# Optimization experiments

Hardware: AMD Instinct MI355X
Metric: run time of the kernel (lower is better)

## Reference

```python
import jax, jax.numpy as jnp
import numpy as np

H = 16
D_MODEL = 1024
D_K = D_MODEL // H
NWORDS = 16384


def setup_inputs() -> dict:
    key0 = jax.random.key(0)
    ks = jax.random.split(key0, 11)
    s = 0.02
    return {
        "query": jax.random.normal(ks[0], (1, D_MODEL), dtype=jnp.float32),
        "key": jax.random.normal(ks[1], (NWORDS, D_MODEL), dtype=jnp.float32),
        "value": jax.random.normal(ks[2], (NWORDS, D_MODEL), dtype=jnp.float32),
        "Wq": jax.random.normal(ks[3], (D_MODEL, D_MODEL), dtype=jnp.float32) * s,
        "bq": jax.random.normal(ks[4], (D_MODEL,), dtype=jnp.float32) * s,
        "Wk": jax.random.normal(ks[5], (D_MODEL, D_MODEL), dtype=jnp.float32) * s,
        "bk": jax.random.normal(ks[6], (D_MODEL,), dtype=jnp.float32) * s,
        "Wv": jax.random.normal(ks[7], (D_MODEL, D_MODEL), dtype=jnp.float32) * s,
        "bv": jax.random.normal(ks[8], (D_MODEL,), dtype=jnp.float32) * s,
        "Wo": jax.random.normal(ks[9], (D_MODEL, D_MODEL), dtype=jnp.float32) * s,
        "bo": jax.random.normal(ks[10], (D_MODEL,), dtype=jnp.float32) * s,
    }


def reference(query, key, value, Wq, bq, Wk, bk, Wv, bv, Wo, bo):
    # torch Linear: y = x @ W.T + b
    q = (query @ Wq.T + bq).reshape(H, D_K)          # [h, d_k]  (single query token)
    k = (key @ Wk.T + bk).reshape(-1, H, D_K)        # [n, h, d_k]
    v = (value @ Wv.T + bv).reshape(-1, H, D_K)      # [n, h, d_k]
    # NOTE: original module applies NO 1/sqrt(d_k) scaling.
    scores = jnp.einsum("hd,nhd->hn", q, k)          # [h, n]
    p_attn = jax.nn.softmax(scores, axis=-1)          # dropout p=0 -> no-op
    x = jnp.einsum("hn,nhd->hd", p_attn, v).reshape(1, H * D_K)  # [1, d_model]
    return x @ Wo.T + bo                              # [1, d_model]
```

## Files before the change

kernel.cpp:

```cpp
#include <hip/hip_runtime.h>

#define DM 1024
#define NW 16384

#define OFF_Q    0
#define OFF_C    1024
#define OFF_D0   17408
#define OFF_S    17424
#define OFF_X    17696
#define OFF_W    18720
#define OFF_E    36864
#define OFF_PART 299008

__global__ __launch_bounds__(256) void k_rowdot(const float* __restrict__ W,
                                                const float* __restrict__ v,
                                                const float* __restrict__ b,
                                                float* __restrict__ out) {
  const int wave = (blockIdx.x * 256 + threadIdx.x) >> 6;
  const int lane = threadIdx.x & 63;
  const float* row = W + (size_t)wave * DM + 4 * lane;
  float s = 0.f;
#pragma unroll
  for (int j = 0; j < 4; ++j) {
    float4 a = *(const float4*)(row + j * 256);
    float4 x = *(const float4*)(v + j * 256 + 4 * lane);
    s += a.x * x.x + a.y * x.y + a.z * x.z + a.w * x.w;
  }
#pragma unroll
  for (int off = 32; off; off >>= 1) s += __shfl_xor(s, off, 64);
  if (lane == 0) out[wave] = s + b[wave];
}

__global__ __launch_bounds__(256) void k_ck(const float* __restrict__ Wk,
                                            const float* __restrict__ bk,
                                            const float* __restrict__ q,
                                            float* __restrict__ c,
                                            float* __restrict__ d0) {
  const int h = blockIdx.x >> 2;
  const int mc = blockIdx.x & 3;
  const int m = mc * 256 + threadIdx.x;
  __shared__ float qh[64];
  if (threadIdx.x < 64) qh[threadIdx.x] = q[h * 64 + threadIdx.x];
  __syncthreads();
  const float* Wp = Wk + (size_t)(h * 64) * DM + m;
  float s = 0.f;
#pragma unroll 8
  for (int d = 0; d < 64; ++d) s += qh[d] * Wp[(size_t)d * DM];
  c[h * DM + m] = s;
  if (mc == 0 && threadIdx.x == 0) {
    float t = 0.f;
    for (int d = 0; d < 64; ++d) t += qh[d] * bk[h * 64 + d];
    d0[h] = t;
  }
}

__global__ __launch_bounds__(256, 3) void k_scores(const float* __restrict__ key,
                                                   const float* __restrict__ c,
                                                   const float* __restrict__ d0,
                                                   float* __restrict__ e,
                                                   float* __restrict__ S) {
  const int lane = threadIdx.x & 63;
  const int wv = threadIdx.x >> 6;
  const int hbase = wv * 4;
  const int n0 = blockIdx.x * 16;
  float4 cf[4][4];
#pragma unroll
  for (int hh = 0; hh < 4; ++hh)
#pragma unroll
    for (int j = 0; j < 4; ++j)
      cf[hh][j] = *(const float4*)(c + (size_t)(hbase + hh) * DM + j * 256 + 4 * lane);
  const int hl = (lane >> 4) & 3;
  const float dh = d0[hbase + hl];
  const bool hi5 = (lane & 32) != 0;
  const bool hi4 = (lane & 16) != 0;
  const bool writer = (lane & 15) == 0;
  float Ssum = 0.f;
  for (int r = 0; r < 16; ++r) {
    const int n = n0 + r;
    const float* kp = key + (size_t)n * DM + 4 * lane;
    float4 k0 = *(const float4*)(kp + 0);
    float4 k1 = *(const float4*)(kp + 256);
    float4 k2 = *(const float4*)(kp + 512);
    float4 k3 = *(const float4*)(kp + 768);
    float s[4];
#pragma unroll
    for (int hh = 0; hh < 4; ++hh) {
      s[hh] = cf[hh][0].x * k0.x + cf[hh][0].y * k0.y + cf[hh][0].z * k0.z + cf[hh][0].w * k0.w
            + cf[hh][1].x * k1.x + cf[hh][1].y * k1.y + cf[hh][1].z * k1.z + cf[hh][1].w * k1.w
            + cf[hh][2].x * k2.x + cf[hh][2].y * k2.y + cf[hh][2].z * k2.z + cf[hh][2].w * k2.w
            + cf[hh][3].x * k3.x + cf[hh][3].y * k3.y + cf[hh][3].z * k3.z + cf[hh][3].w * k3.w;
    }
    float keep0 = hi5 ? s[2] : s[0], send0 = hi5 ? s[0] : s[2];
    float v0 = keep0 + __shfl_xor(send0, 32, 64);
    float keep1 = hi5 ? s[3] : s[1], send1 = hi5 ? s[1] : s[3];
    float v1 = keep1 + __shfl_xor(send1, 32, 64);
    float keep = hi4 ? v1 : v0, send = hi4 ? v0 : v1;
    float t = keep + __shfl_xor(send, 16, 64);
    t += __shfl_xor(t, 8, 64);
    t += __shfl_xor(t, 4, 64);
    t += __shfl_xor(t, 2, 64);
    t += __shfl_xor(t, 1, 64);
    t = __expf(t + dh);
    if (writer) {
      e[(size_t)n * 16 + hbase + hl] = t;
      Ssum += t;
    }
  }
  if (writer) atomicAdd(S + (size_t)(hbase + hl) * 16, Ssum);
}

__global__ __launch_bounds__(256, 4) void k_pv(const float* __restrict__ value,
                                               const float* __restrict__ e,
                                               float* __restrict__ part) {
  const int nb = blockIdx.x >> 2;
  const int mc = blockIdx.x & 3;
  const int col = mc * 256 + threadIdx.x;
  const int n0 = nb * 128;
  float acc[16];
#pragma unroll
  for (int h = 0; h < 16; ++h) acc[h] = 0.f;
  const float* vp = value + (size_t)n0 * DM + col;
  const float* ep = e + (size_t)n0 * 16;
#pragma unroll 2
  for (int r = 0; r < 128; ++r) {
    float v = vp[(size_t)r * DM];
    const float* __restrict__ er = ep + r * 16;
#pragma unroll
    for (int h = 0; h < 16; ++h) acc[h] = fmaf(er[h], v, acc[h]);
  }
  float* pp = part + (size_t)nb * (16 * DM) + col;
#pragma unroll
  for (int h = 0; h < 16; ++h) pp[(size_t)h * DM] = acc[h];
}

__global__ __launch_bounds__(256) void k_wred(const float* __restrict__ part,
                                              float* __restrict__ w) {
  const int o = blockIdx.x * 256 + threadIdx.x;
  float s = 0.f;
#pragma unroll 8
  for (int nb = 0; nb < 128; ++nb) s += part[(size_t)nb * 16384 + o];
  w[o] = s;
}

__global__ __launch_bounds__(256) void k_xproj(const float* __restrict__ Wv,
                                               const float* __restrict__ w,
                                               const float* __restrict__ bv,
                                               const float* __restrict__ S,
                                               float* __restrict__ x) {
  const int wave = (blockIdx.x * 256 + threadIdx.x) >> 6;
  const int lane = threadIdx.x & 63;
  const int h = wave >> 6;
  const float* vec = w + (size_t)h * DM;
  const float* row = Wv + (size_t)wave * DM + 4 * lane;
  float s = 0.f;
#pragma unroll
  for (int j = 0; j < 4; ++j) {
    float4 a = *(const float4*)(row + j * 256);
    float4 x4 = *(const float4*)(vec + j * 256 + 4 * lane);
    s += a.x * x4.x + a.y * x4.y + a.z * x4.z + a.w * x4.w;
  }
#pragma unroll
  for (int off = 32; off; off >>= 1) s += __shfl_xor(s, off, 64);
  if (lane == 0) x[wave] = s / S[(size_t)h * 16] + bv[wave];
}

extern "C" void kernel_launch(void* const* d_in, const int* in_sizes, int n_in,
                              void* d_out, int out_size, void* d_ws, size_t ws_size,
                              hipStream_t stream) {
  const float* query = (const float*)d_in[0];
  const float* key   = (const float*)d_in[1];
  const float* value = (const float*)d_in[2];
  const float* Wq    = (const float*)d_in[3];
  const float* bq    = (const float*)d_in[4];
  const float* Wk    = (const float*)d_in[5];
  const float* bk    = (const float*)d_in[6];
  const float* Wv    = (const float*)d_in[7];
  const float* bv    = (const float*)d_in[8];
  const float* Wo    = (const float*)d_in[9];
  const float* bo    = (const float*)d_in[10];
  float* out = (float*)d_out;
  float* ws  = (float*)d_ws;

  hipMemsetAsync(ws + OFF_S, 0, 256 * sizeof(float), stream);
  k_rowdot <<<256, 256, 0, stream>>>(Wq, query, bq, ws + OFF_Q);
  k_ck     <<<64,  256, 0, stream>>>(Wk, bk, ws + OFF_Q, ws + OFF_C, ws + OFF_D0);
  k_scores <<<1024,256, 0, stream>>>(key, ws + OFF_C, ws + OFF_D0, ws + OFF_E, ws + OFF_S);
  k_pv     <<<512, 256, 0, stream>>>(value, ws + OFF_E, ws + OFF_PART);
  k_wred   <<<64,  256, 0, stream>>>(ws + OFF_PART, ws + OFF_W);
  k_xproj  <<<256, 256, 0, stream>>>(Wv, ws + OFF_W, bv, ws + OFF_S, ws + OFF_X);
  k_rowdot <<<256, 256, 0, stream>>>(Wo, ws + OFF_X, bo, out);
}
```

Baseline: 247.1 us.

## Fuse Q projection into c-vector kernel, restructure PV tiling, widen reduction

Folds the Wq projection and the S zeroing into the k_ck kernel, removing a memset and one launch, though each of the 64 blocks now recomputes its head's 64 q entries. The PV kernel switches to float4 columns with four waves each covering 32 rows of a 128-row chunk, reduced through shared memory, so value loads are wider and the e reads are amortised over four columns. The partial-sum reduction uses four threads per output with shuffle combining, giving 256 blocks instead of 64 for more parallelism.

Result: slower. 259.9 us (+5.1%).

```diff
diff --git a/kernel.cpp b/kernel.cpp
--- a/kernel.cpp
+++ b/kernel.cpp
@@ -3,7 +3,6 @@
 #define DM 1024
 #define NW 16384
 
-#define OFF_Q    0
 #define OFF_C    1024
 #define OFF_D0   17408
 #define OFF_S    17424
@@ -31,26 +30,50 @@
   if (lane == 0) out[wave] = s + b[wave];
 }
 
-__global__ __launch_bounds__(256) void k_ck(const float* __restrict__ Wk,
-                                            const float* __restrict__ bk,
-                                            const float* __restrict__ q,
-                                            float* __restrict__ c,
-                                            float* __restrict__ d0) {
+__global__ __launch_bounds__(256) void k_qck(const float* __restrict__ Wq,
+                                             const float* __restrict__ bq,
+                                             const float* __restrict__ query,
+                                             const float* __restrict__ Wk,
+                                             const float* __restrict__ bk,
+                                             float* __restrict__ c,
+                                             float* __restrict__ d0,
+                                             float* __restrict__ S) {
   const int h = blockIdx.x >> 2;
   const int mc = blockIdx.x & 3;
-  const int m = mc * 256 + threadIdx.x;
+  const int t = threadIdx.x;
+  const int lane = t & 63;
+  const int wv = t >> 6;
   __shared__ float qh[64];
-  if (threadIdx.x < 64) qh[threadIdx.x] = q[h * 64 + threadIdx.x];
-  __syncthreads();
+  if (blockIdx.x == 0 && t < 16) S[t * 16] = 0.f;
+  float4 qv[4];
+#pragma unroll
+  for (int j = 0; j < 4; ++j) qv[j] = *(const float4*)(query + j * 256 + 4 * lane);
+#pragma unroll 1
+  for (int i = 0; i < 16; ++i) {
+    const int d = 4 * i + wv;
+    const int R = h * 64 + d;
+    const float* row = Wq + (size_t)R * DM + 4 * lane;
+    float s = 0.f;
+#pragma unroll
+    for (int j = 0; j < 4; ++j) {
+      float4 a = *(const float4*)(row + j * 256);
+      s += a.x * qv[j].x + a.y * qv[j].y + a.z * qv[j].z + a.w * qv[j].w;
+    }
+#pragma unroll
+    for (int off = 32; off; off >>= 1) s += __shfl_xor(s, off, 64);
+    if (lane == 0) qh[d] = s + bq[R];
+  }
+  __syncthreads();
+  const int m = mc * 256 + t;
   const float* Wp = Wk + (size_t)(h * 64) * DM + m;
   float s = 0.f;
 #pragma unroll 8
   for (int d = 0; d < 64; ++d) s += qh[d] * Wp[(size_t)d * DM];
   c[h * DM + m] = s;
-  if (mc == 0 && threadIdx.x == 0) {
-    float t = 0.f;
-    for (int d = 0; d < 64; ++d) t += qh[d] * bk[h * 64 + d];
-    d0[h] = t;
+  if (mc == 0 && t == 0) {
+    float tt = 0.f;
+    for (int d = 0; d < 64; ++d) tt += qh[d] * bk[h * 64 + d];
+    d0[h] = tt;
   }
 }
 
@@ -109,37 +132,74 @@
   if (writer) atomicAdd(S + (size_t)(hbase + hl) * 16, Ssum);
 }
 
-__global__ __launch_bounds__(256, 4) void k_pv(const float* __restrict__ value,
+__global__ __launch_bounds__(256, 2) void k_pv(const float* __restrict__ value,
                                                const float* __restrict__ e,
                                                float* __restrict__ part) {
   const int nb = blockIdx.x >> 2;
   const int mc = blockIdx.x & 3;
-  const int col = mc * 256 + threadIdx.x;
-  const int n0 = nb * 128;
-  float acc[16];
-#pragma unroll
-  for (int h = 0; h < 16; ++h) acc[h] = 0.f;
+  const int lane = threadIdx.x & 63;
+  const int wy = threadIdx.x >> 6;
+  const int col = mc * 256 + lane * 4;
+  const int n0 = nb * 128 + wy * 32;
+  __shared__ float4 red[2][16][64];
+  float4 acc[16];
+#pragma unroll
+  for (int h = 0; h < 16; ++h) acc[h] = make_float4(0.f, 0.f, 0.f, 0.f);
   const float* vp = value + (size_t)n0 * DM + col;
   const float* ep = e + (size_t)n0 * 16;
-#pragma unroll 2
-  for (int r = 0; r < 128; ++r) {
-    float v = vp[(size_t)r * DM];
+#pragma unroll 4
+  for (int r = 0; r < 32; ++r) {
+    float4 v = *(const float4*)(vp + (size_t)r * DM);
     const float* __restrict__ er = ep + r * 16;
 #pragma unroll
-    for (int h = 0; h < 16; ++h) acc[h] = fmaf(er[h], v, acc[h]);
-  }
-  float* pp = part + (size_t)nb * (16 * DM) + col;
-#pragma unroll
-  for (int h = 0; h < 16; ++h) pp[(size_t)h * DM] = acc[h];
+    for (int h = 0; h < 16; ++h) {
+      float p = er[h];
+      acc[h].x = fmaf(p, v.x, acc[h].x);
+      acc[h].y = fmaf(p, v.y, acc[h].y);
+      acc[h].z = fmaf(p, v.z, acc[h].z);
+      acc[h].w = fmaf(p, v.w, acc[h].w);
+    }
+  }
+  if (wy >= 2) {
+#pragma unroll
+    for (int h = 0; h < 16; ++h) red[wy - 2][h][lane] = acc[h];
+  }
+  __syncthreads();
+  if (wy < 2) {
+#pragma unroll
+    for (int h = 0; h < 16; ++h) {
+      float4 o = red[wy][h][lane];
+      acc[h].x += o.x; acc[h].y += o.y; acc[h].z += o.z; acc[h].w += o.w;
+    }
+  }
+  __syncthreads();
+  if (wy == 1) {
+#pragma unroll
+    for (int h = 0; h < 16; ++h) red[0][h][lane] = acc[h];
+  }
+  __syncthreads();
+  if (wy == 0) {
+    float* pp = part + (size_t)nb * (16 * DM) + col;
+#pragma unroll
+    for (int h = 0; h < 16; ++h) {
+      float4 o = red[0][h][lane];
+      acc[h].x += o.x; acc[h].y += o.y; acc[h].z += o.z; acc[h].w += o.w;
+      *(float4*)(pp + (size_t)h * DM) = acc[h];
+    }
+  }
 }
 
 __global__ __launch_bounds__(256) void k_wred(const float* __restrict__ part,
                                               float* __restrict__ w) {
-  const int o = blockIdx.x * 256 + threadIdx.x;
+  const int gid = blockIdx.x * 256 + threadIdx.x;
+  const int o = gid >> 2;
+  const int q = gid & 3;
   float s = 0.f;
 #pragma unroll 8
-  for (int nb = 0; nb < 128; ++nb) s += part[(size_t)nb * 16384 + o];
-  w[o] = s;
+  for (int i = 0; i < 32; ++i) s += part[(size_t)(q * 32 + i) * 16384 + o];
+  s += __shfl_xor(s, 1, 64);
+  s += __shfl_xor(s, 2, 64);
+  if (q == 0) w[o] = s;
 }
 
 __global__ __launch_bounds__(256) void k_xproj(const float* __restrict__ Wv,
@@ -181,12 +241,10 @@
   float* out = (float*)d_out;
   float* ws  = (float*)d_ws;
 
-  hipMemsetAsync(ws + OFF_S, 0, 256 * sizeof(float), stream);
-  k_rowdot <<<256, 256, 0, stream>>>(Wq, query, bq, ws + OFF_Q);
-  k_ck     <<<64,  256, 0, stream>>>(Wk, bk, ws + OFF_Q, ws + OFF_C, ws + OFF_D0);
+  k_qck    <<<64,  256, 0, stream>>>(Wq, bq, query, Wk, bk, ws + OFF_C, ws + OFF_D0, ws + OFF_S);
   k_scores <<<1024,256, 0, stream>>>(key, ws + OFF_C, ws + OFF_D0, ws + OFF_E, ws + OFF_S);
   k_pv     <<<512, 256, 0, stream>>>(value, ws + OFF_E, ws + OFF_PART);
-  k_wred   <<<64,  256, 0, stream>>>(ws + OFF_PART, ws + OFF_W);
+  k_wred   <<<256, 256, 0, stream>>>(ws + OFF_PART, ws + OFF_W);
   k_xproj  <<<256, 256, 0, stream>>>(Wv, ws + OFF_W, bv, ws + OFF_S, ws + OFF_X);
   k_rowdot <<<256, 256, 0, stream>>>(Wo, ws + OFF_X, bo, out);
 }
```
